# Performance work log

Hardware: AMD Instinct MI355X
Metric: run time of the kernel (lower is better)

The kernel has to match this reference:

```python
import jax, jax.numpy as jnp
import numpy as np

B, N, D, H = 256, 32768, 1024, 16
DH = D // H

def setup_inputs() -> dict:
    key = jax.random.key(0)
    ks = jax.random.split(key, 6)
    scale = 1.0 / np.sqrt(D)  # xavier-ish scale for weights
    return {
        "q": jax.random.normal(ks[0], (B, D), jnp.float32),
        "k": jax.random.normal(ks[1], (N, D), jnp.float32),
        "v": jax.random.normal(ks[2], (N, D), jnp.float32),
        "W_q": jax.random.normal(ks[3], (D, D), jnp.float32) * scale,
        "W_k": jax.random.normal(ks[4], (D, D), jnp.float32) * scale,
        "W_v": jax.random.normal(ks[5], (D, D), jnp.float32) * scale,
    }

def reference(q, k, v, W_q, W_k, W_v):
    # nn.Linear(x) = x @ W.T (no bias)
    qh = (q @ W_q.T).reshape(B, H, DH)   # [B,H,dh]
    kh = (k @ W_k.T).reshape(N, H, DH)   # [N,H,dh]
    vh = (v @ W_v.T).reshape(N, H, DH)   # [N,H,dh]
    inv_sqrt_dh = 1.0 / np.sqrt(DH).astype(np.float32)
    # decode-style cross attention: single query per (head, batch) over N keys
    score = jnp.einsum('bhd,nhd->hbn', qh, kh) * inv_sqrt_dh  # [H,B,N]
    weights = jax.nn.softmax(score, axis=-1)                   # [H,B,N]
    # dropout is identity in eval mode
    context = jnp.einsum('hbn,nhd->bhd', weights, vh)          # [B,H,dh]
    return context.reshape(B, D)
```

## Files before the change

kernel.cpp:

```cpp
#include <hip/hip_runtime.h>
#include <hip/hip_bf16.h>

#define B_  256
#define N_  32768
#define D_  1024
#define H_  16
#define DH_ 64
#define KSPLIT 64
#define STRIPE (N_ / KSPLIT)

typedef __attribute__((ext_vector_type(8))) short bf16x8;
typedef __attribute__((ext_vector_type(4))) float f32x4;

static __device__ __forceinline__ short f2bf(float f) {
    union { __hip_bfloat16 h; short s; } u;
    u.h = __float2bfloat16(f);
    return u.s;
}

static __device__ __forceinline__ bf16x8 pack8(float4 a, float4 b) {
    bf16x8 r;
    r[0] = f2bf(a.x); r[1] = f2bf(a.y); r[2] = f2bf(a.z); r[3] = f2bf(a.w);
    r[4] = f2bf(b.x); r[5] = f2bf(b.y); r[6] = f2bf(b.z); r[7] = f2bf(b.w);
    return r;
}

static __device__ __forceinline__ void gload16(const void* g, void* l) {
    __builtin_amdgcn_global_load_lds(
        (const __attribute__((address_space(1))) void*)g,
        (__attribute__((address_space(3))) void*)l, 16, 0, 0);
}

__global__ __launch_bounds__(256)
void f2b_kernel(const float* __restrict__ in, short* __restrict__ out, int n8)
{
    int i = blockIdx.x * 256 + threadIdx.x;
    if (i < n8) {
        float4 a = ((const float4*)in)[2 * i];
        float4 b = ((const float4*)in)[2 * i + 1];
        ((bf16x8*)out)[i] = pack8(a, b);
    }
}

template<bool SWAP>
__global__ __launch_bounds__(256, 2)
void gemm_fb(const float* __restrict__ A, const short* __restrict__ Bw,
             short* __restrict__ C, int MP, int MQ, int K, int ldc, float alpha)
{
    __shared__ __align__(16) short As_[128 * 32];
    __shared__ __align__(16) short Bs_[128 * 32];

    const int tid  = threadIdx.x;
    const int wave = tid >> 6;
    const int lane = tid & 63;
    const int quad = lane >> 4;
    const int l16  = lane & 15;

    const int gp = MP >> 7, gq = MQ >> 7;
    const int bid = blockIdx.x;
    int bp, bq;
    if (gp >= 8) {
        int xcd = bid & 7, w = bid >> 3, sp = gp >> 3;
        bp = xcd * sp + w / gq;
        bq = w % gq;
    } else { bp = bid / gq; bq = bid % gq; }

    const int wm = (wave & 1) * 64;
    const int wn = (wave >> 1) * 64;

    const char* gB[2]; char* lB[2];
    const float* gA[2]; char* lA[2];
#pragma unroll
    for (int j = 0; j < 2; ++j) {
        int s = j * 256 + tid;
        int r = s >> 2, g = s & 3;
        gB[j] = (const char*)(Bw + (size_t)(bq * 128 + r) * K) + g * 16;
        lB[j] = (char*)Bs_ + s * 16;
        gA[j] = A + (size_t)(bp * 128 + r) * K + g * 8;
        lA[j] = (char*)As_ + s * 16;
    }

    const short* tileA = SWAP ? Bs_ : As_;
    const short* tileB = SWAP ? As_ : Bs_;

    f32x4 acc[4][4];
#pragma unroll
    for (int i = 0; i < 4; ++i)
#pragma unroll
        for (int j = 0; j < 4; ++j) acc[i][j] = (f32x4){0.f, 0.f, 0.f, 0.f};

    for (int kt = 0; kt < K; kt += 32) {
        __syncthreads();
#pragma unroll
        for (int j = 0; j < 2; ++j) { gload16(gB[j], lB[j]); gB[j] += 64; }
        float4 a0[2], a1[2];
#pragma unroll
        for (int j = 0; j < 2; ++j) {
            a0[j] = *(const float4*)(gA[j]);
            a1[j] = *(const float4*)(gA[j] + 4);
            gA[j] += 32;
        }
#pragma unroll
        for (int j = 0; j < 2; ++j)
            *(bf16x8*)lA[j] = pack8(a0[j], a1[j]);
        __syncthreads();

        bf16x8 af[4], bf[4];
#pragma unroll
        for (int f = 0; f < 4; ++f) {
            af[f] = *(const bf16x8*)&tileA[(wm + f * 16 + l16) * 32 + quad * 8];
            bf[f] = *(const bf16x8*)&tileB[(wn + f * 16 + l16) * 32 + quad * 8];
        }
#pragma unroll
        for (int mi = 0; mi < 4; ++mi)
#pragma unroll
            for (int ni = 0; ni < 4; ++ni)
                acc[mi][ni] = __builtin_amdgcn_mfma_f32_16x16x32_bf16(
                    af[mi], bf[ni], acc[mi][ni], 0, 0, 0);
    }

    const int rb = (SWAP ? bq : bp) * 128;
    const int cb = (SWAP ? bp : bq) * 128;
#pragma unroll
    for (int mi = 0; mi < 4; ++mi)
#pragma unroll
        for (int ni = 0; ni < 4; ++ni)
#pragma unroll
            for (int reg = 0; reg < 4; ++reg) {
                int r = rb + wm + mi * 16 + quad * 4 + reg;
                int c = cb + wn + ni * 16 + l16;
                C[(size_t)r * ldc + c] = f2bf(acc[mi][ni][reg] * alpha);
            }
}

__global__ __launch_bounds__(256, 2)
void attn_kernel(const short* __restrict__ qh, const short* __restrict__ kh,
                 const short* __restrict__ vhT, float* __restrict__ partO,
                 float* __restrict__ partM, float* __restrict__ partL)
{
    const int st = blockIdx.x, h = blockIdx.y;
    const int tid  = threadIdx.x;
    const int wave = tid >> 6;
    const int lane = tid & 63;
    const int quad = lane >> 4;
    const int l16  = lane & 15;

    __shared__ __align__(16) short Ps[4][32][72];

    const int hoff = h * DH_;

    bf16x8 qfr[2][2][2];
#pragma unroll
    for (int qb2 = 0; qb2 < 2; ++qb2)
#pragma unroll
        for (int qf = 0; qf < 2; ++qf)
#pragma unroll
            for (int ks = 0; ks < 2; ++ks)
                qfr[qb2][qf][ks] = *(const bf16x8*)
                    (qh + (size_t)(qb2 * 128 + wave * 32 + qf * 16 + l16) * D_
                        + hoff + ks * 32 + quad * 8);

    f32x4 ofrag[2][2][4];
    float m_i[2][2], l_i[2][2];
#pragma unroll
    for (int qb2 = 0; qb2 < 2; ++qb2)
#pragma unroll
        for (int qf = 0; qf < 2; ++qf) {
            m_i[qb2][qf] = -__builtin_inff();
            l_i[qb2][qf] = 0.f;
#pragma unroll
            for (int dt = 0; dt < 4; ++dt) ofrag[qb2][qf][dt] = (f32x4){0.f,0.f,0.f,0.f};
        }

    const int n0 = st * STRIPE;

    for (int ch = 0; ch < STRIPE; ch += 64) {
        const int nb = n0 + ch;

        bf16x8 akf[4][2], avf[4][2];
#pragma unroll
        for (int kf = 0; kf < 4; ++kf)
#pragma unroll
            for (int ks = 0; ks < 2; ++ks)
                akf[kf][ks] = *(const bf16x8*)(kh + (size_t)(nb + kf * 16 + l16) * D_
                                               + hoff + ks * 32 + quad * 8);
#pragma unroll
        for (int dt = 0; dt < 4; ++dt)
#pragma unroll
            for (int g = 0; g < 2; ++g)
                avf[dt][g] = *(const bf16x8*)(vhT + (size_t)(hoff + dt * 16 + l16) * N_
                                              + nb + g * 32 + quad * 8);

#pragma unroll
        for (int qb2 = 0; qb2 < 2; ++qb2) {
            f32x4 sf[4][2];
#pragma unroll
            for (int kf = 0; kf < 4; ++kf)
#pragma unroll
                for (int qf = 0; qf < 2; ++qf) sf[kf][qf] = (f32x4){0.f,0.f,0.f,0.f};
#pragma unroll
            for (int ks = 0; ks < 2; ++ks)
#pragma unroll
                for (int kf = 0; kf < 4; ++kf)
#pragma unroll
                    for (int qf = 0; qf < 2; ++qf)
                        sf[kf][qf] = __builtin_amdgcn_mfma_f32_16x16x32_bf16(
                            akf[kf][ks], qfr[qb2][qf][ks], sf[kf][qf], 0, 0, 0);

#pragma unroll
            for (int qf = 0; qf < 2; ++qf) {
                float mx = sf[0][qf][0];
#pragma unroll
                for (int kf = 0; kf < 4; ++kf)
#pragma unroll
                    for (int r = 0; r < 4; ++r) mx = fmaxf(mx, sf[kf][qf][r]);
                mx = fmaxf(mx, __shfl_xor(mx, 16));
                mx = fmaxf(mx, __shfl_xor(mx, 32));
                const float mold = m_i[qb2][qf];
                if (!__all(mx - mold <= 8.f)) {
                    float mn = fmaxf(mold, mx);
                    float al = exp2f(mold - mn);
                    m_i[qb2][qf] = mn;
                    l_i[qb2][qf] *= al;
#pragma unroll
                    for (int dt = 0; dt < 4; ++dt) ofrag[qb2][qf][dt] *= al;
                }
                const float mn = m_i[qb2][qf];
                float ps = 0.f;
#pragma unroll
                for (int kf = 0; kf < 4; ++kf) {
                    float p0 = exp2f(sf[kf][qf][0] - mn);
                    float p1 = exp2f(sf[kf][qf][1] - mn);
                    float p2 = exp2f(sf[kf][qf][2] - mn);
                    float p3 = exp2f(sf[kf][qf][3] - mn);
                    ps += (p0 + p1) + (p2 + p3);
                    *(short4*)&Ps[wave][qf * 16 + l16][kf * 16 + quad * 4] =
                        make_short4(f2bf(p0), f2bf(p1), f2bf(p2), f2bf(p3));
                }
                ps += __shfl_xor(ps, 16);
                ps += __shfl_xor(ps, 32);
                l_i[qb2][qf] += ps;
            }

#pragma unroll
            for (int qf = 0; qf < 2; ++qf)
#pragma unroll
                for (int g = 0; g < 2; ++g) {
                    bf16x8 bP = *(const bf16x8*)&Ps[wave][qf * 16 + l16][g * 32 + quad * 8];
#pragma unroll
                    for (int dt = 0; dt < 4; ++dt)
                        ofrag[qb2][qf][dt] = __builtin_amdgcn_mfma_f32_16x16x32_bf16(
                            avf[dt][g], bP, ofrag[qb2][qf][dt], 0, 0, 0);
                }
        }
    }

    const int pid = (h * KSPLIT + st) * 4 + wave;
#pragma unroll
    for (int qb2 = 0; qb2 < 2; ++qb2) {
        const size_t rowb = (size_t)(pid * 2 + qb2) * 32;
#pragma unroll
        for (int qf = 0; qf < 2; ++qf)
#pragma unroll
            for (int dt = 0; dt < 4; ++dt)
                *(f32x4*)&partO[(rowb + qf * 16 + l16) * 64 + dt * 16 + quad * 4]
                    = ofrag[qb2][qf][dt];
        if (quad == 0)
#pragma unroll
            for (int qf = 0; qf < 2; ++qf) {
                partM[rowb + qf * 16 + l16] = m_i[qb2][qf];
                partL[rowb + qf * 16 + l16] = l_i[qb2][qf];
            }
    }
}

__global__ __launch_bounds__(256)
void merge_kernel(const float* __restrict__ partO, const float* __restrict__ partM,
                  const float* __restrict__ partL, float* __restrict__ out)
{
    int idx = blockIdx.x * 256 + threadIdx.x;
    int b   = idx >> 10;
    int col = idx & 1023;
    int h   = col >> 6;
    int d   = col & 63;
    int qb2 = b >> 7, rr = b & 127;
    int w = rr >> 5, rin = rr & 31;

    float mmax = -__builtin_inff();
#pragma unroll
    for (int st = 0; st < KSPLIT; ++st) {
        int slot = (((h * KSPLIT + st) * 4 + w) * 2 + qb2) * 32 + rin;
        mmax = fmaxf(mmax, partM[slot]);
    }
    float L = 0.f, o = 0.f;
#pragma unroll
    for (int st = 0; st < KSPLIT; ++st) {
        int slot = (((h * KSPLIT + st) * 4 + w) * 2 + qb2) * 32 + rin;
        float c = exp2f(partM[slot] - mmax);
        L += c * partL[slot];
        o += c * partO[(size_t)slot * 64 + d];
    }
    out[idx] = o / L;
}

extern "C" void kernel_launch(void* const* d_in, const int* in_sizes, int n_in,
                              void* d_out, int out_size, void* d_ws, size_t ws_size,
                              hipStream_t stream) {
    const float* q   = (const float*)d_in[0];
    const float* k   = (const float*)d_in[1];
    const float* v   = (const float*)d_in[2];
    const float* W_q = (const float*)d_in[3];
    const float* W_k = (const float*)d_in[4];
    const float* W_v = (const float*)d_in[5];
    float* out = (float*)d_out;

    short* qh  = (short*)d_ws;
    short* kh  = qh  + (size_t)B_ * D_;
    short* vhT = kh  + (size_t)N_ * D_;
    float* partO = (float*)(vhT + (size_t)D_ * N_);
    float* partM = partO + (size_t)H_ * KSPLIT * 4 * 2 * 32 * 64;
    float* partL = partM + (size_t)H_ * KSPLIT * 4 * 2 * 32;
    short* Wqb = (short*)(partL + (size_t)H_ * KSPLIT * 4 * 2 * 32);
    short* Wkb = Wqb + (size_t)D_ * D_;
    short* Wvb = Wkb + (size_t)D_ * D_;

    dim3 blk(256);
    const int w8 = (D_ * D_) / 8;
    const float alpha_q = 0.125f * 1.4426950408889634f;

    f2b_kernel<<<dim3(w8 / 256), blk, 0, stream>>>(W_q, Wqb, w8);
    f2b_kernel<<<dim3(w8 / 256), blk, 0, stream>>>(W_k, Wkb, w8);
    f2b_kernel<<<dim3(w8 / 256), blk, 0, stream>>>(W_v, Wvb, w8);

    gemm_fb<false><<<dim3(2 * 8), blk, 0, stream>>>(q, Wqb, qh, B_, D_, D_, D_, alpha_q);

    gemm_fb<false><<<dim3(256 * 8), blk, 0, stream>>>(k, Wkb, kh, N_, D_, D_, D_, 1.0f);

    gemm_fb<true><<<dim3(256 * 8), blk, 0, stream>>>(v, Wvb, vhT, N_, D_, D_, N_, 1.0f);

    attn_kernel<<<dim3(KSPLIT, H_), blk, 0, stream>>>(qh, kh, vhT, partO, partM, partL);
    merge_kernel<<<dim3((B_ * D_) / 256), blk, 0, stream>>>(partO, partM, partL, out);
}
```

Before: 694.3 us.

## Load GEMM operand fragments directly from global memory, dropping LDS staging

The projection GEMM no longer stages A and B tiles through shared memory with two barriers per k-step. Each wave now loads its own MFMA fragments straight from global memory, converting fp32 activations to bf16 in registers. This removes the LDS traffic and the block synchronisation. In exchange, data shared between waves is no longer reused on-chip, so global and L2 traffic per block goes up (each fragment is fetched by two waves), and the per-lane global loads are strided rather than coalesced.

```diff
diff --git a/kernel.cpp b/kernel.cpp
--- a/kernel.cpp
+++ b/kernel.cpp
@@ -23,12 +23,6 @@
     r[0] = f2bf(a.x); r[1] = f2bf(a.y); r[2] = f2bf(a.z); r[3] = f2bf(a.w);
     r[4] = f2bf(b.x); r[5] = f2bf(b.y); r[6] = f2bf(b.z); r[7] = f2bf(b.w);
     return r;
-}
-
-static __device__ __forceinline__ void gload16(const void* g, void* l) {
-    __builtin_amdgcn_global_load_lds(
-        (const __attribute__((address_space(1))) void*)g,
-        (__attribute__((address_space(3))) void*)l, 16, 0, 0);
 }
 
 __global__ __launch_bounds__(256)
@@ -47,9 +41,6 @@
 void gemm_fb(const float* __restrict__ A, const short* __restrict__ Bw,
              short* __restrict__ C, int MP, int MQ, int K, int ldc, float alpha)
 {
-    __shared__ __align__(16) short As_[128 * 32];
-    __shared__ __align__(16) short Bs_[128 * 32];
-
     const int tid  = threadIdx.x;
     const int wave = tid >> 6;
     const int lane = tid & 63;
@@ -68,20 +59,18 @@
     const int wm = (wave & 1) * 64;
     const int wn = (wave >> 1) * 64;
 
-    const char* gB[2]; char* lB[2];
-    const float* gA[2]; char* lA[2];
-#pragma unroll
-    for (int j = 0; j < 2; ++j) {
-        int s = j * 256 + tid;
-        int r = s >> 2, g = s & 3;
-        gB[j] = (const char*)(Bw + (size_t)(bq * 128 + r) * K) + g * 16;
-        lB[j] = (char*)Bs_ + s * 16;
-        gA[j] = A + (size_t)(bp * 128 + r) * K + g * 8;
-        lA[j] = (char*)As_ + s * 16;
-    }
-
-    const short* tileA = SWAP ? Bs_ : As_;
-    const short* tileB = SWAP ? As_ : Bs_;
+    const int ar = (SWAP ? bq : bp) * 128 + wm;
+    const int br = (SWAP ? bp : bq) * 128 + wn;
+
+    const float* pf[4];
+    const short* pw[4];
+#pragma unroll
+    for (int f = 0; f < 4; ++f) {
+        const int frow = (SWAP ? br : ar) + f * 16 + l16;
+        const int wrow = (SWAP ? ar : br) + f * 16 + l16;
+        pf[f] = A  + (size_t)frow * K + quad * 8;
+        pw[f] = Bw + (size_t)wrow * K + quad * 8;
+    }
 
     f32x4 acc[4][4];
 #pragma unroll
@@ -90,45 +79,41 @@
         for (int j = 0; j < 4; ++j) acc[i][j] = (f32x4){0.f, 0.f, 0.f, 0.f};
 
     for (int kt = 0; kt < K; kt += 32) {
-        __syncthreads();
-#pragma unroll
-        for (int j = 0; j < 2; ++j) { gload16(gB[j], lB[j]); gB[j] += 64; }
-        float4 a0[2], a1[2];
-#pragma unroll
-        for (int j = 0; j < 2; ++j) {
-            a0[j] = *(const float4*)(gA[j]);
-            a1[j] = *(const float4*)(gA[j] + 4);
-            gA[j] += 32;
+        float4 x[4], y[4];
+#pragma unroll
+        for (int f = 0; f < 4; ++f) {
+            x[f] = *(const float4*)(pf[f]);
+            y[f] = *(const float4*)(pf[f] + 4);
+            pf[f] += 32;
         }
-#pragma unroll
-        for (int j = 0; j < 2; ++j)
-            *(bf16x8*)lA[j] = pack8(a0[j], a1[j]);
-        __syncthreads();
-
-        bf16x8 af[4], bf[4];
+        bf16x8 wfr[4];
 #pragma unroll
         for (int f = 0; f < 4; ++f) {
-            af[f] = *(const bf16x8*)&tileA[(wm + f * 16 + l16) * 32 + quad * 8];
-            bf[f] = *(const bf16x8*)&tileB[(wn + f * 16 + l16) * 32 + quad * 8];
+            wfr[f] = *(const bf16x8*)(pw[f]);
+            pw[f] += 32;
         }
+        bf16x8 cfr[4];
+#pragma unroll
+        for (int f = 0; f < 4; ++f) cfr[f] = pack8(x[f], y[f]);
+
 #pragma unroll
         for (int mi = 0; mi < 4; ++mi)
 #pragma unroll
             for (int ni = 0; ni < 4; ++ni)
                 acc[mi][ni] = __builtin_amdgcn_mfma_f32_16x16x32_bf16(
-                    af[mi], bf[ni], acc[mi][ni], 0, 0, 0);
-    }
-
-    const int rb = (SWAP ? bq : bp) * 128;
-    const int cb = (SWAP ? bp : bq) * 128;
+                    SWAP ? wfr[mi] : cfr[mi],
+                    SWAP ? cfr[ni] : wfr[ni],
+                    acc[mi][ni], 0, 0, 0);
+    }
+
 #pragma unroll
     for (int mi = 0; mi < 4; ++mi)
 #pragma unroll
         for (int ni = 0; ni < 4; ++ni)
 #pragma unroll
             for (int reg = 0; reg < 4; ++reg) {
-                int r = rb + wm + mi * 16 + quad * 4 + reg;
-                int c = cb + wn + ni * 16 + l16;
+                int r = ar + mi * 16 + quad * 4 + reg;
+                int c = br + ni * 16 + l16;
                 C[(size_t)r * ldc + c] = f2bf(acc[mi][ni][reg] * alpha);
             }
 }
```

Result: slower. 1.313 ms (+89.1%).

## Enlarge projection GEMM tiles to 256x256 with double-buffered, swizzled LDS

Applied to the files above, without the earlier changes.

Rewrites the fp32-input projection GEMM to use 256x256 output tiles with 512 threads and a K-step of 64. Shared-memory staging is double-buffered so the next tile's global loads overlap the current MFMA work, and an XOR swizzle is applied to the LDS layout to avoid bank conflicts. The larger tiles raise arithmetic reuse per loaded byte. The costs are 128KB of LDS and a 128-float accumulator per thread, which may limit occupancy. The Q projection now launches only 4 blocks.

```diff
diff --git a/kernel.cpp b/kernel.cpp
--- a/kernel.cpp
+++ b/kernel.cpp
@@ -43,12 +43,12 @@
 }
 
 template<bool SWAP>
-__global__ __launch_bounds__(256, 2)
+__global__ __launch_bounds__(512, 2)
 void gemm_fb(const float* __restrict__ A, const short* __restrict__ Bw,
              short* __restrict__ C, int MP, int MQ, int K, int ldc, float alpha)
 {
-    __shared__ __align__(16) short As_[128 * 32];
-    __shared__ __align__(16) short Bs_[128 * 32];
+    __shared__ __align__(16) short As_[2][256 * 64];
+    __shared__ __align__(16) short Bs_[2][256 * 64];
 
     const int tid  = threadIdx.x;
     const int wave = tid >> 6;
@@ -56,7 +56,7 @@
     const int quad = lane >> 4;
     const int l16  = lane & 15;
 
-    const int gp = MP >> 7, gq = MQ >> 7;
+    const int gp = MP >> 8, gq = MQ >> 8;
     const int bid = blockIdx.x;
     int bp, bq;
     if (gp >= 8) {
@@ -65,71 +65,98 @@
         bq = w % gq;
     } else { bp = bid / gq; bq = bid % gq; }
 
-    const int wm = (wave & 1) * 64;
-    const int wn = (wave >> 1) * 64;
-
-    const char* gB[2]; char* lB[2];
-    const float* gA[2]; char* lA[2];
-#pragma unroll
-    for (int j = 0; j < 2; ++j) {
-        int s = j * 256 + tid;
-        int r = s >> 2, g = s & 3;
-        gB[j] = (const char*)(Bw + (size_t)(bq * 128 + r) * K) + g * 16;
-        lB[j] = (char*)Bs_ + s * 16;
-        gA[j] = A + (size_t)(bp * 128 + r) * K + g * 8;
-        lA[j] = (char*)As_ + s * 16;
-    }
-
-    const short* tileA = SWAP ? Bs_ : As_;
-    const short* tileB = SWAP ? As_ : Bs_;
-
-    f32x4 acc[4][4];
-#pragma unroll
-    for (int i = 0; i < 4; ++i)
-#pragma unroll
-        for (int j = 0; j < 4; ++j) acc[i][j] = (f32x4){0.f, 0.f, 0.f, 0.f};
-
-    for (int kt = 0; kt < K; kt += 32) {
+    const int wm = (wave >> 2) * 128;
+    const int wn = (wave & 3) * 64;
+
+    const float* pA[4];
+    const char*  pB[4];
+    int lofs[4];
+#pragma unroll
+    for (int j = 0; j < 4; ++j) {
+        int s = j * 512 + tid, r = s >> 3, cs = s & 7, cg = cs ^ (r & 7);
+        pA[j]   = A + (size_t)(bp * 256 + r) * K + cg * 8;
+        pB[j]   = (const char*)(Bw + (size_t)(bq * 256 + r) * K + cg * 8);
+        lofs[j] = s * 16;
+    }
+
+    f32x4 acc[8][4];
+#pragma unroll
+    for (int m = 0; m < 8; ++m)
+#pragma unroll
+        for (int n = 0; n < 4; ++n) acc[m][n] = (f32x4){0.f, 0.f, 0.f, 0.f};
+
+#pragma unroll
+    for (int j = 0; j < 4; ++j) { gload16(pB[j], (char*)Bs_[0] + lofs[j]); pB[j] += 128; }
+    {
+        float4 x[4], y[4];
+#pragma unroll
+        for (int j = 0; j < 4; ++j) {
+            x[j] = *(const float4*)(pA[j]);
+            y[j] = *(const float4*)(pA[j] + 4);
+            pA[j] += 64;
+        }
+#pragma unroll
+        for (int j = 0; j < 4; ++j)
+            *(bf16x8*)((char*)As_[0] + lofs[j]) = pack8(x[j], y[j]);
+    }
+    __syncthreads();
+
+    int buf = 0;
+    for (int kt = 0; kt < K; kt += 64) {
+        const int  nb   = buf ^ 1;
+        const bool more = (kt + 64) < K;
+
+        float4 x[4], y[4];
+        if (more) {
+#pragma unroll
+            for (int j = 0; j < 4; ++j) { gload16(pB[j], (char*)Bs_[nb] + lofs[j]); pB[j] += 128; }
+#pragma unroll
+            for (int j = 0; j < 4; ++j) {
+                x[j] = *(const float4*)(pA[j]);
+                y[j] = *(const float4*)(pA[j] + 4);
+                pA[j] += 64;
+            }
+        }
+
+        const short* rowT = SWAP ? Bs_[buf] : As_[buf];
+        const short* colT = SWAP ? As_[buf] : Bs_[buf];
+#pragma unroll
+        for (int ks = 0; ks < 2; ++ks) {
+            const int sw = ((ks * 4 + quad) ^ (l16 & 7)) * 16;
+            bf16x8 cf[4];
+#pragma unroll
+            for (int n = 0; n < 4; ++n)
+                cf[n] = *(const bf16x8*)((const char*)colT + (wn + n * 16 + l16) * 128 + sw);
+#pragma unroll
+            for (int m = 0; m < 8; ++m) {
+                bf16x8 rf = *(const bf16x8*)((const char*)rowT + (wm + m * 16 + l16) * 128 + sw);
+#pragma unroll
+                for (int n = 0; n < 4; ++n)
+                    acc[m][n] = __builtin_amdgcn_mfma_f32_16x16x32_bf16(
+                        rf, cf[n], acc[m][n], 0, 0, 0);
+            }
+        }
+
+        if (more) {
+#pragma unroll
+            for (int j = 0; j < 4; ++j)
+                *(bf16x8*)((char*)As_[nb] + lofs[j]) = pack8(x[j], y[j]);
+        }
         __syncthreads();
-#pragma unroll
-        for (int j = 0; j < 2; ++j) { gload16(gB[j], lB[j]); gB[j] += 64; }
-        float4 a0[2], a1[2];
-#pragma unroll
-        for (int j = 0; j < 2; ++j) {
-            a0[j] = *(const float4*)(gA[j]);
-            a1[j] = *(const float4*)(gA[j] + 4);
-            gA[j] += 32;
-        }
-#pragma unroll
-        for (int j = 0; j < 2; ++j)
-            *(bf16x8*)lA[j] = pack8(a0[j], a1[j]);
-        __syncthreads();
-
-        bf16x8 af[4], bf[4];
-#pragma unroll
-        for (int f = 0; f < 4; ++f) {
-            af[f] = *(const bf16x8*)&tileA[(wm + f * 16 + l16) * 32 + quad * 8];
-            bf[f] = *(const bf16x8*)&tileB[(wn + f * 16 + l16) * 32 + quad * 8];
-        }
-#pragma unroll
-        for (int mi = 0; mi < 4; ++mi)
-#pragma unroll
-            for (int ni = 0; ni < 4; ++ni)
-                acc[mi][ni] = __builtin_amdgcn_mfma_f32_16x16x32_bf16(
-                    af[mi], bf[ni], acc[mi][ni], 0, 0, 0);
-    }
-
-    const int rb = (SWAP ? bq : bp) * 128;
-    const int cb = (SWAP ? bp : bq) * 128;
-#pragma unroll
-    for (int mi = 0; mi < 4; ++mi)
-#pragma unroll
-        for (int ni = 0; ni < 4; ++ni)
+        buf = nb;
+    }
+
+    const int rb = (SWAP ? bq : bp) * 256 + wm;
+    const int cb = (SWAP ? bp : bq) * 256 + wn;
+#pragma unroll
+    for (int m = 0; m < 8; ++m)
+#pragma unroll
+        for (int n = 0; n < 4; ++n)
 #pragma unroll
             for (int reg = 0; reg < 4; ++reg) {
-                int r = rb + wm + mi * 16 + quad * 4 + reg;
-                int c = cb + wn + ni * 16 + l16;
-                C[(size_t)r * ldc + c] = f2bf(acc[mi][ni][reg] * alpha);
+                int r = rb + m * 16 + quad * 4 + reg;
+                int c = cb + n * 16 + l16;
+                C[(size_t)r * ldc + c] = f2bf(acc[m][n][reg] * alpha);
             }
 }
 
@@ -324,7 +351,7 @@
     short* Wkb = Wqb + (size_t)D_ * D_;
     short* Wvb = Wkb + (size_t)D_ * D_;
 
-    dim3 blk(256);
+    dim3 blk(256), blkG(512);
     const int w8 = (D_ * D_) / 8;
     const float alpha_q = 0.125f * 1.4426950408889634f;
 
@@ -332,11 +359,11 @@
     f2b_kernel<<<dim3(w8 / 256), blk, 0, stream>>>(W_k, Wkb, w8);
     f2b_kernel<<<dim3(w8 / 256), blk, 0, stream>>>(W_v, Wvb, w8);
 
-    gemm_fb<false><<<dim3(2 * 8), blk, 0, stream>>>(q, Wqb, qh, B_, D_, D_, D_, alpha_q);
-
-    gemm_fb<false><<<dim3(256 * 8), blk, 0, stream>>>(k, Wkb, kh, N_, D_, D_, D_, 1.0f);
-
-    gemm_fb<true><<<dim3(256 * 8), blk, 0, stream>>>(v, Wvb, vhT, N_, D_, D_, N_, 1.0f);
+    gemm_fb<false><<<dim3(1 * 4), blkG, 0, stream>>>(q, Wqb, qh, B_, D_, D_, D_, alpha_q);
+
+    gemm_fb<false><<<dim3(128 * 4), blkG, 0, stream>>>(k, Wkb, kh, N_, D_, D_, D_, 1.0f);
+
+    gemm_fb<true><<<dim3(128 * 4), blkG, 0, stream>>>(v, Wvb, vhT, N_, D_, D_, N_, 1.0f);
 
     attn_kernel<<<dim3(KSPLIT, H_), blk, 0, stream>>>(qh, kh, vhT, partO, partM, partL);
     merge_kernel<<<dim3((B_ * D_) / 256), blk, 0, stream>>>(partO, partM, partL, out);
```

Measured after the change: 593.5 us. -14.5%, faster.
